# Optimization experiments

Measured on AMD Instinct MI355X. Metric: run time of the kernel, lower is better.

## Reference

```python
import jax, jax.numpy as jnp
import numpy as np

DIM = 512
NUM_HEADS = 8
HEAD_DIM = DIM // NUM_HEADS
SCALE = HEAD_DIM ** -0.5


def setup_inputs() -> dict:
    key = jax.random.key(0)
    k1, k2, k3, k4 = jax.random.split(key, 4)
    x = jax.random.normal(k1, (4, 2048, DIM), dtype=jnp.float32)
    W_qkv = jax.random.normal(k2, (DIM, 3 * DIM), dtype=jnp.float32) * (DIM ** -0.5)
    W_proj = jax.random.normal(k3, (DIM, DIM), dtype=jnp.float32) * (DIM ** -0.5)
    b_proj = jax.random.normal(k4, (DIM,), dtype=jnp.float32) * 0.01
    return {"x": x, "W_qkv": W_qkv, "W_proj": W_proj, "b_proj": b_proj}


def reference(x, W_qkv, W_proj, b_proj):
    B, N, C = x.shape
    H, hd = NUM_HEADS, HEAD_DIM
    # qkv: [B, N, 3, H, hd] -> (q, k, v) each [B, H, N, hd]
    qkv = (x @ W_qkv).reshape(B, N, 3, H, hd)
    qkv = jnp.transpose(qkv, (2, 0, 3, 1, 4))
    q, k, v = qkv[0], qkv[1], qkv[2]
    # eager attention: [B, H, N, N]
    attn = jnp.einsum('bhnd,bhmd->bhnm', q, k) * SCALE
    attn = jax.nn.softmax(attn, axis=-1)
    out = jnp.einsum('bhnm,bhmd->bhnd', attn, v)  # [B, H, N, hd]
    out = jnp.transpose(out, (0, 2, 1, 3)).reshape(B, N, C)
    out = out @ W_proj + b_proj
    return (out, k, v)
```

## Files before the change

### kernel.cpp

```cpp
#include <hip/hip_runtime.h>

typedef unsigned short ushort_t;
typedef __bf16 bf16x8 __attribute__((ext_vector_type(8)));
typedef __bf16 bf16x4 __attribute__((ext_vector_type(4)));
typedef ushort_t u16x8 __attribute__((ext_vector_type(8)));
typedef float f32x4 __attribute__((ext_vector_type(4)));

#define MFMA(a, b, c) __builtin_amdgcn_mfma_f32_16x16x32_bf16(a, b, c, 0, 0, 0)

#if __has_builtin(__builtin_amdgcn_mfma_f32_16x16x16bf16_1k)
typedef short s16x4 __attribute__((ext_vector_type(4)));
__device__ __forceinline__ f32x4 mfma16(bf16x4 a, bf16x4 b, f32x4 c) {
    union { bf16x4 v; s16x4 s; } ua, ub; ua.v = a; ub.v = b;
    return __builtin_amdgcn_mfma_f32_16x16x16bf16_1k(ua.s, ub.s, c, 0, 0, 0);
}
#define MFMA16_ASM 0
#elif __has_builtin(__builtin_amdgcn_mfma_f32_16x16x16_bf16)
__device__ __forceinline__ f32x4 mfma16(bf16x4 a, bf16x4 b, f32x4 c) {
    return __builtin_amdgcn_mfma_f32_16x16x16_bf16(a, b, c, 0, 0, 0);
}
#define MFMA16_ASM 0
#else
__device__ __forceinline__ f32x4 mfma16(bf16x4 a, bf16x4 b, f32x4 c) {
    asm("v_mfma_f32_16x16x16_bf16 %0, %1, %2, %0" : "+v"(c) : "v"(a), "v"(b));
    return c;
}
#define MFMA16_ASM 1
#endif

#define N_X      4194304L
#define N_WQKV   786432L
#define N_WPROJ  262144L
#define OUT_OFF_K 4194304L
#define OUT_OFF_V 8388608L

#define OFF_FLAG   0UL
#define OFF_XB     1024UL
#define OFF_WQKVT  (OFF_XB + 8388608UL)
#define OFF_WPROJT (OFF_WQKVT + 1572864UL)
#define OFF_BPROJ  (OFF_WPROJT + 524288UL)
#define OFF_QB     (OFF_BPROJ + 2048UL)
#define OFF_KB     (OFF_QB + 8388608UL)
#define OFF_VTB    (OFF_KB + 8388608UL)
#define OFF_ATTN   (OFF_VTB + 8388608UL)

#define QSCALE 0.180336880519191f

__device__ __forceinline__ ushort_t f2b(float f) {
    union { float f; unsigned u; } v; v.f = f;
    return (ushort_t)((v.u + 0x7FFFu + ((v.u >> 16) & 1u)) >> 16);
}
__device__ __forceinline__ ushort_t f2b_trunc(float f) {
    union { float f; unsigned u; } v; v.f = f;
    return (ushort_t)(v.u >> 16);
}
__device__ __forceinline__ float b2f(ushort_t h) {
    union { unsigned u; float f; } v; v.u = ((unsigned)h) << 16;
    return v.f;
}
__device__ __forceinline__ float ldf(const float* p, long i) { return p[i]; }
__device__ __forceinline__ float ldf(const ushort_t* p, long i) { return b2f(p[i]); }
__device__ __forceinline__ void stf(float* p, long i, float v) { p[i] = v; }
__device__ __forceinline__ void stf(ushort_t* p, long i, float v) { p[i] = f2b(v); }

__device__ __forceinline__ float fast_exp2(float x) {
#if __has_builtin(__builtin_amdgcn_exp2f)
    return __builtin_amdgcn_exp2f(x);
#else
    return __expf(x * 0.6931471805599453f);
#endif
}

__device__ __forceinline__ void glds16(const void* g, const void* l) {
    __builtin_amdgcn_global_load_lds((__attribute__((address_space(1))) void*)g,
                                     (__attribute__((address_space(3))) void*)l,
                                     16, 0, 0);
}

__global__ void k_detect(const unsigned* __restrict__ x, int* __restrict__ flag) {
    int lane = threadIdx.x & 63;
    int cnt = 0;
#pragma unroll
    for (int i = 0; i < 4; ++i) {
        unsigned w = x[lane + i * 64];
        float v = __uint_as_float((w & 0xFFFFu) << 16);
        float a = fabsf(v);
        if (a > 1e-3f && a < 100.0f) cnt++;
    }
#pragma unroll
    for (int off = 32; off; off >>= 1) cnt += __shfl_down(cnt, off, 64);
    if (lane == 0) *flag = (cnt > 128) ? 1 : 0;
}

template <typename T>
__global__ void k_prep(const T* __restrict__ x, const T* __restrict__ wq,
                       const T* __restrict__ wp, const T* __restrict__ bp,
                       ushort_t* __restrict__ xb, ushort_t* __restrict__ wqT,
                       ushort_t* __restrict__ wpT, float* __restrict__ bpf,
                       const int* __restrict__ flag, int want) {
    if (*flag != want) return;
    long i0 = (long)blockIdx.x * blockDim.x + threadIdx.x;
    long stride = (long)gridDim.x * blockDim.x;
    for (long i = i0; i < N_X; i += stride) xb[i] = f2b(ldf(x, i));
    for (long i = i0; i < N_WQKV; i += stride) {
        long n = i >> 9, k = i & 511;
        wqT[i] = f2b(ldf(wq, k * 1536 + n));
    }
    for (long i = i0; i < N_WPROJ; i += stride) {
        long n = i >> 9, k = i & 511;
        wpT[i] = f2b(ldf(wp, k * 512 + n));
    }
    for (long i = i0; i < 512; i += stride) bpf[i] = ldf(bp, i);
}

template <typename TOUT>
__global__ __launch_bounds__(256, 2)
void k_qkv(const ushort_t* __restrict__ xb, const ushort_t* __restrict__ wqT,
           ushort_t* __restrict__ qb, ushort_t* __restrict__ kb, ushort_t* __restrict__ vb,
           TOUT* __restrict__ kout, TOUT* __restrict__ vout,
           const int* __restrict__ flag, int want) {
    if (*flag != want) return;
    __shared__ __align__(16) ushort_t As[128 * 32];
    __shared__ __align__(16) ushort_t Bs[128 * 32];
    const int tid = threadIdx.x, wave = tid >> 6, lane = tid & 63;
    const int id = blockIdx.x;
    const int xcd = id & 7, g = id >> 3;
    const int bx = xcd * 8 + (g & 7);
    const int by = g >> 3;
    const int tm = bx * 128, tn = by * 128;
    const int wm = (wave >> 1) * 64, wn = (wave & 1) * 64;
    const int l15 = lane & 15, lq = lane >> 4;
    const int srow = lane >> 2, sc = lane & 3;

    f32x4 acc[4][4];
#pragma unroll
    for (int a = 0; a < 4; ++a)
#pragma unroll
        for (int b = 0; b < 4; ++b) acc[a][b] = (f32x4){0.f, 0.f, 0.f, 0.f};

    for (int k0 = 0; k0 < 512; k0 += 32) {
#pragma unroll
        for (int t = 0; t < 2; ++t) {
            int s = wave * 2 + t;
            int row = s * 16 + srow;
            int c = (sc ^ (row >> 1)) & 3;
            glds16(xb  + (long)(tm + row) * 512 + k0 + c * 8, As + s * 512);
            glds16(wqT + (long)(tn + row) * 512 + k0 + c * 8, Bs + s * 512);
        }
        __syncthreads();
        bf16x8 af[4], bfr[4];
#pragma unroll
        for (int mt = 0; mt < 4; ++mt) {
            int row = wm + mt * 16 + l15;
            int cp = (lq ^ (row >> 1)) & 3;
            af[mt] = *(const bf16x8*)(As + row * 32 + cp * 8);
        }
#pragma unroll
        for (int nt = 0; nt < 4; ++nt) {
            int row = wn + nt * 16 + l15;
            int cp = (lq ^ (row >> 1)) & 3;
            bfr[nt] = *(const bf16x8*)(Bs + row * 32 + cp * 8);
        }
#pragma unroll
        for (int mt = 0; mt < 4; ++mt)
#pragma unroll
            for (int nt = 0; nt < 4; ++nt)
                acc[mt][nt] = MFMA(af[mt], bfr[nt], acc[mt][nt]);
        __syncthreads();
    }

#pragma unroll
    for (int mt = 0; mt < 4; ++mt) {
#pragma unroll
        for (int nt = 0; nt < 4; ++nt) {
            int j = tn + wn + nt * 16 + l15;
            int t = j >> 9, h = (j >> 6) & 7, d = j & 63;
#pragma unroll
            for (int r = 0; r < 4; ++r) {
                int mm = tm + wm + mt * 16 + lq * 4 + r;
                int b = mm >> 11, nn = mm & 2047;
                float v = acc[mt][nt][r];
                long idx = ((long)(b * 8 + h) * 2048 + nn) * 64 + d;
                if (t == 0) {
                    qb[idx] = f2b(v * QSCALE);
                } else if (t == 1) {
                    kb[idx] = f2b(v);
                    stf(kout, idx, v);
                } else {
                    vb[idx] = f2b(v);
                    stf(vout, idx, v);
                }
            }
        }
    }
}

__global__ __launch_bounds__(256, 4)
void k_vtrans(const ushort_t* __restrict__ vb, ushort_t* __restrict__ vtb) {
    __shared__ ushort_t T[64 * 64];
    const int tid = threadIdx.x;
    const int bh = blockIdx.y, ktile = blockIdx.x;
    const long base = (long)bh * 131072 + (long)ktile * 64 * 64;
    const int row = tid >> 2, cq = tid & 3;
#pragma unroll
    for (int half = 0; half < 2; ++half) {
        int c = cq + half * 4;
        u16x8 v = *(const u16x8*)(vb + base + row * 64 + c * 8);
#pragma unroll
        for (int e = 0; e < 8; ++e) {
            int dim = c * 8 + e;
            T[row * 64 + ((dim + row) & 63)] = v[e];
        }
    }
    __syncthreads();
#pragma unroll
    for (int it = 0; it < 16; ++it) {
        int d = (tid >> 6) * 16 + it;
        int key = tid & 63;
        vtb[(long)bh * 131072 + (long)d * 2048 + ktile * 64 + key] =
            T[key * 64 + ((d + key) & 63)];
    }
}

__global__ __launch_bounds__(256, 2)
void k_attn(const ushort_t* __restrict__ qb, const ushort_t* __restrict__ kb,
            const ushort_t* __restrict__ vtb, ushort_t* __restrict__ attnb) {
    __shared__ __align__(16) ushort_t Kt[128 * 64];
    __shared__ __align__(16) ushort_t Vt[64 * 128];
    const int tid = threadIdx.x, wave = tid >> 6, lane = tid & 63;
    const int l15 = lane & 15, lq = lane >> 4;
    const int id = blockIdx.x;
    const int xcd = id & 7, g = id >> 3;
    const int bh = xcd * 4 + (g >> 4);
    const int qt = g & 15;
    const long kvbase = (long)bh * 131072;
    const long qbase = kvbase + (long)qt * 128 * 64;

    bf16x8 aQ[2][2];
#pragma unroll
    for (int mq = 0; mq < 2; ++mq)
#pragma unroll
        for (int kt = 0; kt < 2; ++kt)
            aQ[mq][kt] = *(const bf16x8*)(qb + qbase +
                (long)(wave * 32 + mq * 16 + l15) * 64 + kt * 32 + lq * 8);

    f32x4 oacc[2][4];
#pragma unroll
    for (int mq = 0; mq < 2; ++mq)
#pragma unroll
        for (int nd = 0; nd < 4; ++nd) oacc[mq][nd] = (f32x4){0.f, 0.f, 0.f, 0.f};
    float ssum[2] = {0.f, 0.f};

    const int ksrow = lane >> 3, kschunk = lane & 7;
    const int vsrow = lane >> 4, vschunk = lane & 15;

    for (int j = 0; j < 16; ++j) {
#pragma unroll
        for (int t = 0; t < 4; ++t) {
            int s = wave * 4 + t;
            {
                int row = s * 8 + ksrow;
                int c = kschunk ^ (row & 7);
                glds16(kb + kvbase + (long)(j * 128 + row) * 64 + c * 8, Kt + s * 512);
            }
            {
                int row = s * 4 + vsrow;
                int c = vschunk ^ (row & 15);
                glds16(vtb + kvbase + (long)row * 2048 + j * 128 + c * 8, Vt + s * 512);
            }
        }
        __syncthreads();

#pragma unroll
        for (int h = 0; h < 2; ++h) {
            f32x4 sacc[2][4];
#pragma unroll
            for (int mq = 0; mq < 2; ++mq)
#pragma unroll
                for (int nt = 0; nt < 4; ++nt) sacc[mq][nt] = (f32x4){0.f, 0.f, 0.f, 0.f};
#pragma unroll
            for (int nt = 0; nt < 4; ++nt) {
                int krow = h * 64 + nt * 16 + l15;
#pragma unroll
                for (int kt = 0; kt < 2; ++kt) {
                    int c = (kt * 4 + lq) ^ (krow & 7);
                    bf16x8 bk = *(const bf16x8*)(Kt + krow * 64 + c * 8);
                    sacc[0][nt] = MFMA(bk, aQ[0][kt], sacc[0][nt]);
                    sacc[1][nt] = MFMA(bk, aQ[1][kt], sacc[1][nt]);
                }
            }
            bf16x4 pb[2][4];
#pragma unroll
            for (int mq = 0; mq < 2; ++mq) {
#pragma unroll
                for (int nt = 0; nt < 4; ++nt) {
                    union { ushort_t u[4]; bf16x4 v; } pk;
                    float acc0 = 0.f, acc1 = 0.f;
#pragma unroll
                    for (int r = 0; r < 4; ++r) {
                        float p = fast_exp2(sacc[mq][nt][r]);
                        ushort_t tt = f2b_trunc(p);
                        pk.u[r] = tt;
                        if (r & 1) acc1 += b2f(tt); else acc0 += b2f(tt);
                    }
                    ssum[mq] += acc0 + acc1;
                    pb[mq][nt] = pk.v;
                }
            }
#pragma unroll
            for (int nd = 0; nd < 4; ++nd) {
                int drow = nd * 16 + l15;
#pragma unroll
                for (int nt = 0; nt < 4; ++nt) {
                    int kc = h * 8 + nt * 2 + (lq >> 1);
                    int cc = kc ^ (drow & 15);
                    bf16x4 va = *(const bf16x4*)(Vt + drow * 128 + cc * 8 + (lq & 1) * 4);
                    oacc[0][nd] = mfma16(va, pb[0][nt], oacc[0][nd]);
                    oacc[1][nd] = mfma16(va, pb[1][nt], oacc[1][nd]);
                }
            }
        }
        __syncthreads();
    }

#if MFMA16_ASM
    asm volatile("s_nop 7\n\ts_nop 7");
#endif
    const int b = bh >> 3, hh = bh & 7;
#pragma unroll
    for (int mq = 0; mq < 2; ++mq) {
        float s = ssum[mq];
        s += __shfl_xor(s, 16, 64);
        s += __shfl_xor(s, 32, 64);
        float inv = 1.0f / s;
        int n = qt * 128 + wave * 32 + mq * 16 + l15;
        long rowbase = ((long)b * 2048 + n) * 512 + hh * 64;
#pragma unroll
        for (int nd = 0; nd < 4; ++nd) {
            int d0 = nd * 16 + lq * 4;
            union { ushort_t u[4]; unsigned long long ll; } o;
#pragma unroll
            for (int r = 0; r < 4; ++r) o.u[r] = f2b(oacc[mq][nd][r] * inv);
            *(unsigned long long*)(attnb + rowbase + d0) = o.ll;
        }
    }
}

template <typename TOUT>
__global__ __launch_bounds__(256, 2)
void k_proj(const ushort_t* __restrict__ ab, const ushort_t* __restrict__ wpT,
            const float* __restrict__ bpf, TOUT* __restrict__ out,
            const int* __restrict__ flag, int want) {
    if (*flag != want) return;
    __shared__ __align__(16) ushort_t As[128 * 32];
    __shared__ __align__(16) ushort_t Bs[128 * 32];
    const int tid = threadIdx.x, wave = tid >> 6, lane = tid & 63;
    const int id = blockIdx.x;
    const int xcd = id & 7, g = id >> 3;
    const int bx = xcd * 8 + (g & 7);
    const int by = g >> 3;
    const int tm = bx * 128, tn = by * 128;
    const int wm = (wave >> 1) * 64, wn = (wave & 1) * 64;
    const int l15 = lane & 15, lq = lane >> 4;
    const int srow = lane >> 2, sc = lane & 3;

    f32x4 acc[4][4];
#pragma unroll
    for (int a = 0; a < 4; ++a)
#pragma unroll
        for (int b = 0; b < 4; ++b) acc[a][b] = (f32x4){0.f, 0.f, 0.f, 0.f};

    for (int k0 = 0; k0 < 512; k0 += 32) {
#pragma unroll
        for (int t = 0; t < 2; ++t) {
            int s = wave * 2 + t;
            int row = s * 16 + srow;
            int c = (sc ^ (row >> 1)) & 3;
            glds16(ab  + (long)(tm + row) * 512 + k0 + c * 8, As + s * 512);
            glds16(wpT + (long)(tn + row) * 512 + k0 + c * 8, Bs + s * 512);
        }
        __syncthreads();
        bf16x8 af[4], bfr[4];
#pragma unroll
        for (int mt = 0; mt < 4; ++mt) {
            int row = wm + mt * 16 + l15;
            int cp = (lq ^ (row >> 1)) & 3;
            af[mt] = *(const bf16x8*)(As + row * 32 + cp * 8);
        }
#pragma unroll
        for (int nt = 0; nt < 4; ++nt) {
            int row = wn + nt * 16 + l15;
            int cp = (lq ^ (row >> 1)) & 3;
            bfr[nt] = *(const bf16x8*)(Bs + row * 32 + cp * 8);
        }
#pragma unroll
        for (int mt = 0; mt < 4; ++mt)
#pragma unroll
            for (int nt = 0; nt < 4; ++nt)
                acc[mt][nt] = MFMA(af[mt], bfr[nt], acc[mt][nt]);
        __syncthreads();
    }

#pragma unroll
    for (int mt = 0; mt < 4; ++mt) {
#pragma unroll
        for (int nt = 0; nt < 4; ++nt) {
            int j = tn + wn + nt * 16 + l15;
            float bias = bpf[j];
#pragma unroll
            for (int r = 0; r < 4; ++r) {
                int mm = tm + wm + mt * 16 + lq * 4 + r;
                stf(out, (long)mm * 512 + j, acc[mt][nt][r] + bias);
            }
        }
    }
}

extern "C" void kernel_launch(void* const* d_in, const int* in_sizes, int n_in,
                              void* d_out, int out_size, void* d_ws, size_t ws_size,
                              hipStream_t stream) {
    (void)in_sizes; (void)n_in; (void)out_size; (void)ws_size;
    char* ws = (char*)d_ws;
    int* flag = (int*)(ws + OFF_FLAG);
    ushort_t* xb  = (ushort_t*)(ws + OFF_XB);
    ushort_t* wqT = (ushort_t*)(ws + OFF_WQKVT);
    ushort_t* wpT = (ushort_t*)(ws + OFF_WPROJT);
    float*    bpf = (float*)(ws + OFF_BPROJ);
    ushort_t* qb  = (ushort_t*)(ws + OFF_QB);
    ushort_t* kb  = (ushort_t*)(ws + OFF_KB);
    ushort_t* vtb = (ushort_t*)(ws + OFF_VTB);
    ushort_t* ab  = (ushort_t*)(ws + OFF_ATTN);
    ushort_t* vb  = (ushort_t*)(ws + OFF_ATTN);

    k_detect<<<1, 64, 0, stream>>>((const unsigned*)d_in[0], flag);

    k_prep<float><<<1024, 256, 0, stream>>>(
        (const float*)d_in[0], (const float*)d_in[1], (const float*)d_in[2],
        (const float*)d_in[3], xb, wqT, wpT, bpf, flag, 0);
    k_prep<ushort_t><<<1024, 256, 0, stream>>>(
        (const ushort_t*)d_in[0], (const ushort_t*)d_in[1], (const ushort_t*)d_in[2],
        (const ushort_t*)d_in[3], xb, wqT, wpT, bpf, flag, 1);

    k_qkv<float><<<768, 256, 0, stream>>>(xb, wqT, qb, kb, vb,
        (float*)d_out + OUT_OFF_K, (float*)d_out + OUT_OFF_V, flag, 0);
    k_qkv<ushort_t><<<768, 256, 0, stream>>>(xb, wqT, qb, kb, vb,
        (ushort_t*)d_out + OUT_OFF_K, (ushort_t*)d_out + OUT_OFF_V, flag, 1);

    k_vtrans<<<dim3(32, 32), 256, 0, stream>>>(vb, vtb);

    k_attn<<<512, 256, 0, stream>>>(qb, kb, vtb, ab);

    k_proj<float><<<256, 256, 0, stream>>>(ab, wpT, bpf, (float*)d_out, flag, 0);
    k_proj<ushort_t><<<256, 256, 0, stream>>>(ab, wpT, bpf, (ushort_t*)d_out, flag, 1);
}
```

Baseline: 178.1 us.

## Double-buffer LDS in GEMM and attention kernels, inline dtype detection, vectorize prep

Adds double-buffered LDS staging with explicit vmcnt waits to k_qkv, k_attn and k_proj, so global-to-LDS loads for the next tile overlap the MFMA work on the current one. Removes the separate detect kernel and the duplicated flag-gated launches: each kernel now detects the input dtype itself, which cuts the number of launches. Vectorizes the prep conversion to write 8 bf16 values per store. The cost is doubled LDS per block, which may limit occupancy, and hand-placed waitcnt counts that must match the number of loads issued.

Measured after the change: 180.5 us. About the same (+1.3%).

```diff
diff --git a/kernel.cpp b/kernel.cpp
--- a/kernel.cpp
+++ b/kernel.cpp
@@ -58,10 +58,6 @@
     union { unsigned u; float f; } v; v.u = ((unsigned)h) << 16;
     return v.f;
 }
-__device__ __forceinline__ float ldf(const float* p, long i) { return p[i]; }
-__device__ __forceinline__ float ldf(const ushort_t* p, long i) { return b2f(p[i]); }
-__device__ __forceinline__ void stf(float* p, long i, float v) { p[i] = v; }
-__device__ __forceinline__ void stf(ushort_t* p, long i, float v) { p[i] = f2b(v); }
 
 __device__ __forceinline__ float fast_exp2(float x) {
 #if __has_builtin(__builtin_amdgcn_exp2f)
@@ -77,7 +73,7 @@
                                      16, 0, 0);
 }
 
-__global__ void k_detect(const unsigned* __restrict__ x, int* __restrict__ flag) {
+__device__ __forceinline__ int detect_bf16(const unsigned* __restrict__ x) {
     int lane = threadIdx.x & 63;
     int cnt = 0;
 #pragma unroll
@@ -88,40 +84,77 @@
         if (a > 1e-3f && a < 100.0f) cnt++;
     }
 #pragma unroll
-    for (int off = 32; off; off >>= 1) cnt += __shfl_down(cnt, off, 64);
-    if (lane == 0) *flag = (cnt > 128) ? 1 : 0;
-}
-
-template <typename T>
-__global__ void k_prep(const T* __restrict__ x, const T* __restrict__ wq,
-                       const T* __restrict__ wp, const T* __restrict__ bp,
+    for (int off = 1; off < 64; off <<= 1) cnt += __shfl_xor(cnt, off, 64);
+    return cnt > 128;
+}
+
+__global__ void k_prep(const void* __restrict__ xv, const void* __restrict__ wqv,
+                       const void* __restrict__ wpv, const void* __restrict__ bpv,
                        ushort_t* __restrict__ xb, ushort_t* __restrict__ wqT,
-                       ushort_t* __restrict__ wpT, float* __restrict__ bpf,
-                       const int* __restrict__ flag, int want) {
-    if (*flag != want) return;
+                       ushort_t* __restrict__ wpT, float* __restrict__ bpf) {
+    const int isb = detect_bf16((const unsigned*)xv);
     long i0 = (long)blockIdx.x * blockDim.x + threadIdx.x;
     long stride = (long)gridDim.x * blockDim.x;
-    for (long i = i0; i < N_X; i += stride) xb[i] = f2b(ldf(x, i));
-    for (long i = i0; i < N_WQKV; i += stride) {
-        long n = i >> 9, k = i & 511;
-        wqT[i] = f2b(ldf(wq, k * 1536 + n));
-    }
-    for (long i = i0; i < N_WPROJ; i += stride) {
-        long n = i >> 9, k = i & 511;
-        wpT[i] = f2b(ldf(wp, k * 512 + n));
-    }
-    for (long i = i0; i < 512; i += stride) bpf[i] = ldf(bp, i);
-}
-
-template <typename TOUT>
+    if (isb) {
+        const ushort_t* x = (const ushort_t*)xv;
+        const ushort_t* wq = (const ushort_t*)wqv;
+        const ushort_t* wp = (const ushort_t*)wpv;
+        const ushort_t* bp = (const ushort_t*)bpv;
+        for (long i = i0; i < N_X / 8; i += stride)
+            ((u16x8*)xb)[i] = ((const u16x8*)x)[i];
+        for (long i = i0; i < N_WQKV / 8; i += stride) {
+            long n = (i * 8) >> 9, k = (i * 8) & 511;
+            u16x8 o;
+#pragma unroll
+            for (int e = 0; e < 8; ++e) o[e] = wq[(k + e) * 1536 + n];
+            ((u16x8*)wqT)[i] = o;
+        }
+        for (long i = i0; i < N_WPROJ / 8; i += stride) {
+            long n = (i * 8) >> 9, k = (i * 8) & 511;
+            u16x8 o;
+#pragma unroll
+            for (int e = 0; e < 8; ++e) o[e] = wp[(k + e) * 512 + n];
+            ((u16x8*)wpT)[i] = o;
+        }
+        for (long i = i0; i < 512; i += stride) bpf[i] = b2f(bp[i]);
+    } else {
+        const float* x = (const float*)xv;
+        const float* wq = (const float*)wqv;
+        const float* wp = (const float*)wpv;
+        const float* bp = (const float*)bpv;
+        for (long i = i0; i < N_X / 8; i += stride) {
+            f32x4 a = ((const f32x4*)x)[i * 2], b = ((const f32x4*)x)[i * 2 + 1];
+            u16x8 o;
+#pragma unroll
+            for (int e = 0; e < 4; ++e) { o[e] = f2b(a[e]); o[e + 4] = f2b(b[e]); }
+            ((u16x8*)xb)[i] = o;
+        }
+        for (long i = i0; i < N_WQKV / 8; i += stride) {
+            long n = (i * 8) >> 9, k = (i * 8) & 511;
+            u16x8 o;
+#pragma unroll
+            for (int e = 0; e < 8; ++e) o[e] = f2b(wq[(k + e) * 1536 + n]);
+            ((u16x8*)wqT)[i] = o;
+        }
+        for (long i = i0; i < N_WPROJ / 8; i += stride) {
+            long n = (i * 8) >> 9, k = (i * 8) & 511;
+            u16x8 o;
+#pragma unroll
+            for (int e = 0; e < 8; ++e) o[e] = f2b(wp[(k + e) * 512 + n]);
+            ((u16x8*)wpT)[i] = o;
+        }
+        for (long i = i0; i < 512; i += stride) bpf[i] = bp[i];
+    }
+}
+
 __global__ __launch_bounds__(256, 2)
-void k_qkv(const ushort_t* __restrict__ xb, const ushort_t* __restrict__ wqT,
+void k_qkv(const unsigned* __restrict__ xraw,
+           const ushort_t* __restrict__ xb, const ushort_t* __restrict__ wqT,
            ushort_t* __restrict__ qb, ushort_t* __restrict__ kb, ushort_t* __restrict__ vb,
-           TOUT* __restrict__ kout, TOUT* __restrict__ vout,
-           const int* __restrict__ flag, int want) {
-    if (*flag != want) return;
-    __shared__ __align__(16) ushort_t As[128 * 32];
-    __shared__ __align__(16) ushort_t Bs[128 * 32];
+           void* __restrict__ dout) {
+    const int isb = detect_bf16(xraw);
+    __shared__ __align__(16) ushort_t As[2][128 * 32];
+    __shared__ __align__(16) ushort_t Bs[2][128 * 32];
     const int tid = threadIdx.x, wave = tid >> 6, lane = tid & 63;
     const int id = blockIdx.x;
     const int xcd = id & 7, g = id >> 3;
@@ -138,37 +171,59 @@
 #pragma unroll
         for (int b = 0; b < 4; ++b) acc[a][b] = (f32x4){0.f, 0.f, 0.f, 0.f};
 
-    for (int k0 = 0; k0 < 512; k0 += 32) {
+    auto stage = [&](int k0, int buf) {
 #pragma unroll
         for (int t = 0; t < 2; ++t) {
             int s = wave * 2 + t;
             int row = s * 16 + srow;
             int c = (sc ^ (row >> 1)) & 3;
-            glds16(xb  + (long)(tm + row) * 512 + k0 + c * 8, As + s * 512);
-            glds16(wqT + (long)(tn + row) * 512 + k0 + c * 8, Bs + s * 512);
-        }
-        __syncthreads();
+            glds16(xb  + (long)(tm + row) * 512 + k0 + c * 8, &As[buf][s * 512]);
+            glds16(wqT + (long)(tn + row) * 512 + k0 + c * 8, &Bs[buf][s * 512]);
+        }
+    };
+
+    stage(0, 0);
+    for (int ks = 0; ks < 16; ++ks) {
+        int cur = ks & 1;
+        if (ks < 15) {
+            stage((ks + 1) * 32, cur ^ 1);
+            asm volatile("s_waitcnt vmcnt(4)" ::: "memory");
+        } else {
+            asm volatile("s_waitcnt vmcnt(0)" ::: "memory");
+        }
+        __builtin_amdgcn_sched_barrier(0);
+        __builtin_amdgcn_s_barrier();
+
+        const ushort_t* Ac = &As[cur][0];
+        const ushort_t* Bc = &Bs[cur][0];
         bf16x8 af[4], bfr[4];
 #pragma unroll
         for (int mt = 0; mt < 4; ++mt) {
             int row = wm + mt * 16 + l15;
             int cp = (lq ^ (row >> 1)) & 3;
-            af[mt] = *(const bf16x8*)(As + row * 32 + cp * 8);
+            af[mt] = *(const bf16x8*)(Ac + row * 32 + cp * 8);
         }
 #pragma unroll
         for (int nt = 0; nt < 4; ++nt) {
             int row = wn + nt * 16 + l15;
             int cp = (lq ^ (row >> 1)) & 3;
-            bfr[nt] = *(const bf16x8*)(Bs + row * 32 + cp * 8);
+            bfr[nt] = *(const bf16x8*)(Bc + row * 32 + cp * 8);
         }
 #pragma unroll
         for (int mt = 0; mt < 4; ++mt)
 #pragma unroll
             for (int nt = 0; nt < 4; ++nt)
                 acc[mt][nt] = MFMA(af[mt], bfr[nt], acc[mt][nt]);
-        __syncthreads();
-    }
-
+
+        asm volatile("s_waitcnt lgkmcnt(0)" ::: "memory");
+        __builtin_amdgcn_sched_barrier(0);
+        __builtin_amdgcn_s_barrier();
+    }
+
+    float*    koutf = (float*)dout + OUT_OFF_K;
+    float*    voutf = (float*)dout + OUT_OFF_V;
+    ushort_t* koutb = (ushort_t*)dout + OUT_OFF_K;
+    ushort_t* voutb = (ushort_t*)dout + OUT_OFF_V;
 #pragma unroll
     for (int mt = 0; mt < 4; ++mt) {
 #pragma unroll
@@ -185,10 +240,10 @@
                     qb[idx] = f2b(v * QSCALE);
                 } else if (t == 1) {
                     kb[idx] = f2b(v);
-                    stf(kout, idx, v);
+                    if (isb) koutb[idx] = f2b(v); else koutf[idx] = v;
                 } else {
                     vb[idx] = f2b(v);
-                    stf(vout, idx, v);
+                    if (isb) voutb[idx] = f2b(v); else voutf[idx] = v;
                 }
             }
         }
@@ -225,8 +280,8 @@
 __global__ __launch_bounds__(256, 2)
 void k_attn(const ushort_t* __restrict__ qb, const ushort_t* __restrict__ kb,
             const ushort_t* __restrict__ vtb, ushort_t* __restrict__ attnb) {
-    __shared__ __align__(16) ushort_t Kt[128 * 64];
-    __shared__ __align__(16) ushort_t Vt[64 * 128];
+    __shared__ __align__(16) ushort_t Kt[2][128 * 64];
+    __shared__ __align__(16) ushort_t Vt[2][64 * 128];
     const int tid = threadIdx.x, wave = tid >> 6, lane = tid & 63;
     const int l15 = lane & 15, lq = lane >> 4;
     const int id = blockIdx.x;
@@ -236,40 +291,56 @@
     const long kvbase = (long)bh * 131072;
     const long qbase = kvbase + (long)qt * 128 * 64;
 
-    bf16x8 aQ[2][2];
-#pragma unroll
-    for (int mq = 0; mq < 2; ++mq)
-#pragma unroll
-        for (int kt = 0; kt < 2; ++kt)
-            aQ[mq][kt] = *(const bf16x8*)(qb + qbase +
-                (long)(wave * 32 + mq * 16 + l15) * 64 + kt * 32 + lq * 8);
-
-    f32x4 oacc[2][4];
-#pragma unroll
-    for (int mq = 0; mq < 2; ++mq)
-#pragma unroll
-        for (int nd = 0; nd < 4; ++nd) oacc[mq][nd] = (f32x4){0.f, 0.f, 0.f, 0.f};
-    float ssum[2] = {0.f, 0.f};
-
     const int ksrow = lane >> 3, kschunk = lane & 7;
     const int vsrow = lane >> 4, vschunk = lane & 15;
 
-    for (int j = 0; j < 16; ++j) {
+    auto stage = [&](int j, int buf) {
 #pragma unroll
         for (int t = 0; t < 4; ++t) {
             int s = wave * 4 + t;
             {
                 int row = s * 8 + ksrow;
                 int c = kschunk ^ (row & 7);
-                glds16(kb + kvbase + (long)(j * 128 + row) * 64 + c * 8, Kt + s * 512);
+                glds16(kb + kvbase + (long)(j * 128 + row) * 64 + c * 8, &Kt[buf][s * 512]);
             }
             {
                 int row = s * 4 + vsrow;
                 int c = vschunk ^ (row & 15);
-                glds16(vtb + kvbase + (long)row * 2048 + j * 128 + c * 8, Vt + s * 512);
-            }
-        }
-        __syncthreads();
+                glds16(vtb + kvbase + (long)row * 2048 + j * 128 + c * 8, &Vt[buf][s * 512]);
+            }
+        }
+    };
+
+    stage(0, 0);
+
+    bf16x8 aQ[2][2];
+#pragma unroll
+    for (int mq = 0; mq < 2; ++mq)
+#pragma unroll
+        for (int kt = 0; kt < 2; ++kt)
+            aQ[mq][kt] = *(const bf16x8*)(qb + qbase +
+                (long)(wave * 32 + mq * 16 + l15) * 64 + kt * 32 + lq * 8);
+
+    f32x4 oacc[2][4];
+#pragma unroll
+    for (int mq = 0; mq < 2; ++mq)
+#pragma unroll
+        for (int nd = 0; nd < 4; ++nd) oacc[mq][nd] = (f32x4){0.f, 0.f, 0.f, 0.f};
+    float ssum[2] = {0.f, 0.f};
+
+    for (int j = 0; j < 16; ++j) {
+        int cur = j & 1;
+        if (j < 15) {
+            stage(j + 1, cur ^ 1);
+            asm volatile("s_waitcnt vmcnt(8)" ::: "memory");
+        } else {
+            asm volatile("s_waitcnt vmcnt(0)" ::: "memory");
+        }
+        __builtin_amdgcn_sched_barrier(0);
+        __builtin_amdgcn_s_barrier();
+
+        const ushort_t* Ktc = &Kt[cur][0];
+        const ushort_t* Vtc = &Vt[cur][0];
 
 #pragma unroll
         for (int h = 0; h < 2; ++h) {
@@ -284,7 +355,7 @@
 #pragma unroll
                 for (int kt = 0; kt < 2; ++kt) {
                     int c = (kt * 4 + lq) ^ (krow & 7);
-                    bf16x8 bk = *(const bf16x8*)(Kt + krow * 64 + c * 8);
+                    bf16x8 bk = *(const bf16x8*)(Ktc + krow * 64 + c * 8);
                     sacc[0][nt] = MFMA(bk, aQ[0][kt], sacc[0][nt]);
                     sacc[1][nt] = MFMA(bk, aQ[1][kt], sacc[1][nt]);
                 }
@@ -314,13 +385,16 @@
                 for (int nt = 0; nt < 4; ++nt) {
                     int kc = h * 8 + nt * 2 + (lq >> 1);
                     int cc = kc ^ (drow & 15);
-                    bf16x4 va = *(const bf16x4*)(Vt + drow * 128 + cc * 8 + (lq & 1) * 4);
+                    bf16x4 va = *(const bf16x4*)(Vtc + drow * 128 + cc * 8 + (lq & 1) * 4);
                     oacc[0][nd] = mfma16(va, pb[0][nt], oacc[0][nd]);
                     oacc[1][nd] = mfma16(va, pb[1][nt], oacc[1][nd]);
                 }
             }
         }
-        __syncthreads();
+
+        asm volatile("s_waitcnt lgkmcnt(0)" ::: "memory");
+        __builtin_amdgcn_sched_barrier(0);
+        __builtin_amdgcn_s_barrier();
     }
 
 #if MFMA16_ASM
@@ -346,14 +420,13 @@
     }
 }
 
-template <typename TOUT>
 __global__ __launch_bounds__(256, 2)
-void k_proj(const ushort_t* __restrict__ ab, const ushort_t* __restrict__ wpT,
-            const float* __restrict__ bpf, TOUT* __restrict__ out,
-            const int* __restrict__ flag, int want) {
-    if (*flag != want) return;
-    __shared__ __align__(16) ushort_t As[128 * 32];
-    __shared__ __align__(16) ushort_t Bs[128 * 32];
+void k_proj(const unsigned* __restrict__ xraw,
+            const ushort_t* __restrict__ ab, const ushort_t* __restrict__ wpT,
+            const float* __restrict__ bpf, void* __restrict__ dout) {
+    const int isb = detect_bf16(xraw);
+    __shared__ __align__(16) ushort_t As[2][128 * 32];
+    __shared__ __align__(16) ushort_t Bs[2][128 * 32];
     const int tid = threadIdx.x, wave = tid >> 6, lane = tid & 63;
     const int id = blockIdx.x;
     const int xcd = id & 7, g = id >> 3;
@@ -370,35 +443,53 @@
 #pragma unroll
         for (int b = 0; b < 4; ++b) acc[a][b] = (f32x4){0.f, 0.f, 0.f, 0.f};
 
-    for (int k0 = 0; k0 < 512; k0 += 32) {
+    auto stage = [&](int k0, int buf) {
 #pragma unroll
         for (int t = 0; t < 2; ++t) {
             int s = wave * 2 + t;
             int row = s * 16 + srow;
             int c = (sc ^ (row >> 1)) & 3;
-            glds16(ab  + (long)(tm + row) * 512 + k0 + c * 8, As + s * 512);
-            glds16(wpT + (long)(tn + row) * 512 + k0 + c * 8, Bs + s * 512);
-        }
-        __syncthreads();
+            glds16(ab  + (long)(tm + row) * 512 + k0 + c * 8, &As[buf][s * 512]);
+            glds16(wpT + (long)(tn + row) * 512 + k0 + c * 8, &Bs[buf][s * 512]);
+        }
+    };
+
+    stage(0, 0);
+    for (int ks = 0; ks < 16; ++ks) {
+        int cur = ks & 1;
+        if (ks < 15) {
+            stage((ks + 1) * 32, cur ^ 1);
+            asm volatile("s_waitcnt vmcnt(4)" ::: "memory");
+        } else {
+            asm volatile("s_waitcnt vmcnt(0)" ::: "memory");
+        }
+        __builtin_amdgcn_sched_barrier(0);
+        __builtin_amdgcn_s_barrier();
+
+        const ushort_t* Ac = &As[cur][0];
+        const ushort_t* Bc = &Bs[cur][0];
         bf16x8 af[4], bfr[4];
 #pragma unroll
         for (int mt = 0; mt < 4; ++mt) {
             int row = wm + mt * 16 + l15;
             int cp = (lq ^ (row >> 1)) & 3;
-            af[mt] = *(const bf16x8*)(As + row * 32 + cp * 8);
+            af[mt] = *(const bf16x8*)(Ac + row * 32 + cp * 8);
         }
 #pragma unroll
         for (int nt = 0; nt < 4; ++nt) {
             int row = wn + nt * 16 + l15;
             int cp = (lq ^ (row >> 1)) & 3;
-            bfr[nt] = *(const bf16x8*)(Bs + row * 32 + cp * 8);
+            bfr[nt] = *(const bf16x8*)(Bc + row * 32 + cp * 8);
         }
 #pragma unroll
         for (int mt = 0; mt < 4; ++mt)
 #pragma unroll
             for (int nt = 0; nt < 4; ++nt)
                 acc[mt][nt] = MFMA(af[mt], bfr[nt], acc[mt][nt]);
-        __syncthreads();
+
+        asm volatile("s_waitcnt lgkmcnt(0)" ::: "memory");
+        __builtin_amdgcn_sched_barrier(0);
+        __builtin_amdgcn_s_barrier();
     }
 
 #pragma unroll
@@ -410,7 +501,9 @@
 #pragma unroll
             for (int r = 0; r < 4; ++r) {
                 int mm = tm + wm + mt * 16 + lq * 4 + r;
-                stf(out, (long)mm * 512 + j, acc[mt][nt][r] + bias);
+                float v = acc[mt][nt][r] + bias;
+                if (isb) ((ushort_t*)dout)[(long)mm * 512 + j] = f2b(v);
+                else     ((float*)dout)[(long)mm * 512 + j] = v;
             }
         }
     }
@@ -421,7 +514,6 @@
                               hipStream_t stream) {
     (void)in_sizes; (void)n_in; (void)out_size; (void)ws_size;
     char* ws = (char*)d_ws;
-    int* flag = (int*)(ws + OFF_FLAG);
     ushort_t* xb  = (ushort_t*)(ws + OFF_XB);
     ushort_t* wqT = (ushort_t*)(ws + OFF_WQKVT);
     ushort_t* wpT = (ushort_t*)(ws + OFF_WPROJT);
@@ -432,24 +524,15 @@
     ushort_t* ab  = (ushort_t*)(ws + OFF_ATTN);
     ushort_t* vb  = (ushort_t*)(ws + OFF_ATTN);
 
-    k_detect<<<1, 64, 0, stream>>>((const unsigned*)d_in[0], flag);
-
-    k_prep<float><<<1024, 256, 0, stream>>>(
-        (const float*)d_in[0], (const float*)d_in[1], (const float*)d_in[2],
-        (const float*)d_in[3], xb, wqT, wpT, bpf, flag, 0);
-    k_prep<ushort_t><<<1024, 256, 0, stream>>>(
-        (const ushort_t*)d_in[0], (const ushort_t*)d_in[1], (const ushort_t*)d_in[2],
-        (const ushort_t*)d_in[3], xb, wqT, wpT, bpf, flag, 1);
-
-    k_qkv<float><<<768, 256, 0, stream>>>(xb, wqT, qb, kb, vb,
-        (float*)d_out + OUT_OFF_K, (float*)d_out + OUT_OFF_V, flag, 0);
-    k_qkv<ushort_t><<<768, 256, 0, stream>>>(xb, wqT, qb, kb, vb,
-        (ushort_t*)d_out + OUT_OFF_K, (ushort_t*)d_out + OUT_OFF_V, flag, 1);
+    k_prep<<<1024, 256, 0, stream>>>(d_in[0], d_in[1], d_in[2], d_in[3],
+                                     xb, wqT, wpT, bpf);
+
+    k_qkv<<<768, 256, 0, stream>>>((const unsigned*)d_in[0], xb, wqT,
+                                   qb, kb, vb, d_out);
 
     k_vtrans<<<dim3(32, 32), 256, 0, stream>>>(vb, vtb);
 
     k_attn<<<512, 256, 0, stream>>>(qb, kb, vtb, ab);
 
-    k_proj<float><<<256, 256, 0, stream>>>(ab, wpT, bpf, (float*)d_out, flag, 0);
-    k_proj<ushort_t><<<256, 256, 0, stream>>>(ab, wpT, bpf, (ushort_t*)d_out, flag, 1);
-}
+    k_proj<<<256, 256, 0, stream>>>((const unsigned*)d_in[0], ab, wpT, bpf, d_out);
+}
```
